# Optimization experiments

Hardware: AMD Instinct MI355X
Metric: run time of the kernel (lower is better)

## Reference

```python
import jax, jax.numpy as jnp
import numpy as np

D_MODEL = 1024
NUM_HEADS = 16
D_K = D_MODEL // NUM_HEADS


def setup_inputs() -> dict:
    key = jax.random.key(0)
    ks = jax.random.split(key, 12)
    B, S = 2, 2048
    s = 1.0 / np.sqrt(D_MODEL)
    inp = {
        'q': jax.random.normal(ks[0], (B, S, D_MODEL), jnp.float32),
        'k': jax.random.normal(ks[1], (B, S, D_MODEL), jnp.float32),
        'v': jax.random.normal(ks[2], (B, S, D_MODEL), jnp.float32),
        'mask': jax.random.randint(ks[3], (B, S, S), 0, 2, jnp.int32),
        'Wq_w': jax.random.normal(ks[4], (D_MODEL, D_MODEL), jnp.float32) * s,
        'Wq_b': jnp.zeros((D_MODEL,), jnp.float32),
        'Wk_w': jax.random.normal(ks[5], (D_MODEL, D_MODEL), jnp.float32) * s,
        'Wk_b': jnp.zeros((D_MODEL,), jnp.float32),
        'Wv_w': jax.random.normal(ks[6], (D_MODEL, D_MODEL), jnp.float32) * s,
        'Wv_b': jnp.zeros((D_MODEL,), jnp.float32),
        'Wo_w': jax.random.normal(ks[7], (D_MODEL, D_MODEL), jnp.float32) * s,
        'Wo_b': jnp.zeros((D_MODEL,), jnp.float32),
    }
    return inp


def reference(q, k, v, mask, Wq_w, Wq_b, Wk_w, Wk_b, Wv_w, Wv_b, Wo_w, Wo_b):
    B, Sq, _ = q.shape
    # torch Linear: x @ W.T + b
    qp = (q @ Wq_w.T + Wq_b).reshape(B, Sq, NUM_HEADS, D_K)
    kp = (k @ Wk_w.T + Wk_b).reshape(B, k.shape[1], NUM_HEADS, D_K)
    vp = (v @ Wv_w.T + Wv_b).reshape(B, v.shape[1], NUM_HEADS, D_K)
    # scores: [B, H, Sq, Sk]
    scores = jnp.einsum('bqhd,bkhd->bhqk', qp, kp) / np.sqrt(D_K).astype(np.float32)
    scores = jnp.where(mask[:, None, :, :] == 0, jnp.float32(-10000.0), scores)
    attn = jax.nn.softmax(scores, axis=-1)
    ctx = jnp.einsum('bhqk,bkhd->bqhd', attn, vp).reshape(B, Sq, D_MODEL)
    return ctx @ Wo_w.T + Wo_b
```

## Files before the change

### kernel.cpp

```cpp
#include <hip/hip_runtime.h>

#define DM   1024
#define HN   16
#define DKH  64
#define SEQ  2048
#define BATCH 2

typedef __attribute__((ext_vector_type(8))) __bf16 bf16x8;
typedef __attribute__((ext_vector_type(4))) float  f32x4;
typedef __attribute__((ext_vector_type(16))) float f32x16;
typedef __attribute__((ext_vector_type(2)))  int   i32x2;

#define AS1 __attribute__((address_space(1)))
#define AS3 __attribute__((address_space(3)))
#define GLL(g, l) __builtin_amdgcn_global_load_lds((const AS1 unsigned int*)(const void*)(g), \
                                                   (AS3 unsigned int*)(void*)(l), 16, 0, 0)

__device__ __forceinline__ unsigned short f2bf(float f) {
  union { float f; unsigned u; } v; v.f = f;
  unsigned u = v.u;
  u += 0x7FFFu + ((u >> 16) & 1u);
  return (unsigned short)(u >> 16);
}

__global__ __launch_bounds__(256) void prep_kernel(
    const float* __restrict__ q, const float* __restrict__ k,
    const float* __restrict__ v,
    const float* __restrict__ Wq, const float* __restrict__ Wk,
    const float* __restrict__ Wv, const float* __restrict__ Wo,
    const int* __restrict__ mask,
    unsigned short* __restrict__ q_bf, unsigned short* __restrict__ k_bf,
    unsigned short* __restrict__ v_bf,
    unsigned short* __restrict__ Wq_bf, unsigned short* __restrict__ Wk_bf,
    unsigned short* __restrict__ Wv_bf, unsigned short* __restrict__ Wo_bf,
    unsigned* __restrict__ pkm) {
  const int bid = blockIdx.x;
  if (bid < 12288) {
    int t = bid >> 12, r = bid & 4095;
    const float* in = (t == 0) ? q : (t == 1) ? k : v;
    unsigned short* out = (t == 0) ? q_bf : (t == 1) ? k_bf : v_bf;
    int i = r * 256 + threadIdx.x;
    float4 f = ((const float4*)in)[i];
    ushort4 o;
    o.x = f2bf(f.x); o.y = f2bf(f.y); o.z = f2bf(f.z); o.w = f2bf(f.w);
    ((ushort4*)out)[i] = o;
  } else if (bid < 16384) {
    int b2 = bid - 12288;
    int t = b2 >> 10, r = b2 & 1023;
    const float* in = (t == 0) ? Wq : (t == 1) ? Wk : (t == 2) ? Wv : Wo;
    unsigned short* out = (t == 0) ? Wq_bf : (t == 1) ? Wk_bf : (t == 2) ? Wv_bf : Wo_bf;
    int i = r * 256 + threadIdx.x;
    float4 f = ((const float4*)in)[i];
    ushort4 o;
    o.x = f2bf(f.x); o.y = f2bf(f.y); o.z = f2bf(f.z); o.w = f2bf(f.w);
    ((ushort4*)out)[i] = o;
  } else {
    int W = (bid - 16384) * 256 + threadIdx.x;
    const int4* base = (const int4*)(mask + (size_t)(W >> 6) * SEQ + (size_t)(W & 63) * 32);
    unsigned bits = 0;
#pragma unroll
    for (int g = 0; g < 8; ++g) {
      int4 m = base[g];
      bits |= (unsigned)(m.x != 0) << (4 * g);
      bits |= (unsigned)(m.y != 0) << (4 * g + 1);
      bits |= (unsigned)(m.z != 0) << (4 * g + 2);
      bits |= (unsigned)(m.w != 0) << (4 * g + 3);
    }
    pkm[W] = bits;
  }
}

__device__ __forceinline__ void gemm_core_pipe(
    const unsigned short* __restrict__ A,
    const unsigned short* __restrict__ W,
    unsigned short* lds,
    f32x4 (&acc)[4][4]) {
  const int tid = threadIdx.x;
  const int wave = tid >> 6, lane = tid & 63;
  const int l15 = lane & 15, quad = lane >> 4;
  const int wr = wave >> 1, wc = wave & 1;

  const int rl = lane >> 2;
  const int cg = (lane & 3) ^ (((rl & 3) + ((rl >> 2) & 3)) & 3);
  const unsigned short* ga = A + (size_t)(wave * 32 + rl) * DM + cg * 8;
  const unsigned short* gb = W + (size_t)(wave * 32 + rl) * DM + cg * 8;
  unsigned short* la = lds + wave * 1024;
  unsigned short* lb = lds + 4096 + wave * 1024;

  const int cfr = (quad ^ (((l15 & 3) + ((l15 >> 2) & 3)) & 3)) * 8;

  auto stage = [&](int ki, int sb) {
    const unsigned short* a = ga + ki * 32;
    const unsigned short* b = gb + ki * 32;
    GLL(a, la + sb);                    GLL(a + (size_t)16 * DM, la + sb + 512);
    GLL(b, lb + sb);                    GLL(b + (size_t)16 * DM, lb + sb + 512);
  };
  auto compute = [&](int sb) {
    const unsigned short* Ab = lds + sb;
    const unsigned short* Bb = lds + sb + 4096;
    bf16x8 af[4], bfr[4];
#pragma unroll
    for (int mt = 0; mt < 4; ++mt)
      af[mt] = *(const bf16x8*)(Ab + (size_t)(wr * 64 + mt * 16 + l15) * 32 + cfr);
#pragma unroll
    for (int nt = 0; nt < 4; ++nt)
      bfr[nt] = *(const bf16x8*)(Bb + (size_t)(wc * 64 + nt * 16 + l15) * 32 + cfr);
#pragma unroll
    for (int mt = 0; mt < 4; ++mt)
#pragma unroll
      for (int nt = 0; nt < 4; ++nt)
        acc[mt][nt] = __builtin_amdgcn_mfma_f32_16x16x32_bf16(af[mt], bfr[nt], acc[mt][nt], 0, 0, 0);
  };

  stage(0, 0);
  stage(1, 8192);
  int sb0 = 0, sb1 = 8192, sb2 = 16384;
#pragma unroll 1
  for (int i = 0; i < DM / 32 - 2; ++i) {
    stage(i + 2, sb2);
    asm volatile("s_waitcnt vmcnt(8)\ns_barrier" ::: "memory");
    compute(sb0);
    asm volatile("s_barrier" ::: "memory");
    int t = sb0; sb0 = sb1; sb1 = sb2; sb2 = t;
  }
  asm volatile("s_waitcnt vmcnt(4)\ns_barrier" ::: "memory");
  compute(sb0);
  asm volatile("s_waitcnt vmcnt(0)\ns_barrier" ::: "memory");
  compute(sb1);
}

__global__ __launch_bounds__(256, 3) void gemm_qkv(
    const unsigned short* __restrict__ Aq, const unsigned short* __restrict__ Ak,
    const unsigned short* __restrict__ Av,
    const unsigned short* __restrict__ Wq, const unsigned short* __restrict__ Wk,
    const unsigned short* __restrict__ Wv,
    const float* __restrict__ bq, const float* __restrict__ bk,
    const float* __restrict__ bv,
    unsigned short* __restrict__ oq, unsigned short* __restrict__ ok,
    unsigned short* __restrict__ ovT) {
  const int z = blockIdx.z;
  const unsigned short* A = (z == 0) ? Aq : (z == 1) ? Ak : Av;
  const unsigned short* W = (z == 0) ? Wq : (z == 1) ? Wk : Wv;
  const float* bias = (z == 0) ? bq : (z == 1) ? bk : bv;

  __shared__ __align__(16) unsigned short lds[24576];

  const int bn = blockIdx.x * 128, bm = blockIdx.y * 128;
  f32x4 acc[4][4] = {};
  gemm_core_pipe(A + (size_t)bm * DM, W + (size_t)bn * DM, lds, acc);

  const int tid = threadIdx.x;
  const int wave = tid >> 6, lane = tid & 63;
  const int l15 = lane & 15, quad = lane >> 4;
  const int wr = wave >> 1, wc = wave & 1;

  if (z != 2) {
    const float qs = (z == 0) ? 0.125f * 1.44269504088896f : 1.0f;
    unsigned short* out = (z == 0) ? oq : ok;
#pragma unroll
    for (int mt = 0; mt < 4; ++mt)
#pragma unroll
      for (int nt = 0; nt < 4; ++nt) {
        int col = bn + wc * 64 + nt * 16 + l15;
        float bb = bias[col];
#pragma unroll
        for (int r = 0; r < 4; ++r) {
          int row = bm + wr * 64 + mt * 16 + quad * 4 + r;
          out[(size_t)row * DM + col] = f2bf((acc[mt][nt][r] + bb) * qs);
        }
      }
  } else {
    unsigned short* LT = lds;
    __syncthreads();
#pragma unroll
    for (int mt = 0; mt < 4; ++mt)
#pragma unroll
      for (int nt = 0; nt < 4; ++nt) {
        int c = wc * 64 + nt * 16 + l15;
        float bb = bias[bn + c];
        int t0 = wr * 64 + mt * 16 + quad * 4;
        ushort4 w4;
        w4.x = f2bf(acc[mt][nt][0] + bb);
        w4.y = f2bf(acc[mt][nt][1] + bb);
        w4.z = f2bf(acc[mt][nt][2] + bb);
        w4.w = f2bf(acc[mt][nt][3] + bb);
        *(ushort4*)(LT + (size_t)c * 136 + t0) = w4;
      }
    __syncthreads();
    const int b = bm >> 11, sbase = bm & (SEQ - 1);
#pragma unroll
    for (int j = 0; j < 8; ++j) {
      int c = wave * 32 + (j >> 1) * 8 + (lane >> 3);
      int tk = (j & 1) * 64 + (lane & 7) * 8;
      bf16x8 vv = *(const bf16x8*)(LT + (size_t)c * 136 + tk);
      int C = bn + c;
      int h = C >> 6, dk = C & 63;
      *(bf16x8*)(ovT + ((size_t)((b * HN + h) * DKH + dk)) * SEQ + sbase + tk) = vv;
    }
  }
}

__global__ __launch_bounds__(256, 3) void gemm_wo(
    const unsigned short* __restrict__ A, const unsigned short* __restrict__ W,
    const float* __restrict__ bias, float* __restrict__ out) {
  __shared__ __align__(16) unsigned short lds[24576];

  const int bn = blockIdx.x * 128, bm = blockIdx.y * 128;
  f32x4 acc[4][4] = {};
  gemm_core_pipe(A + (size_t)bm * DM, W + (size_t)bn * DM, lds, acc);

  const int tid = threadIdx.x;
  const int wave = tid >> 6, lane = tid & 63;
  const int l15 = lane & 15, quad = lane >> 4;
  const int wr = wave >> 1, wc = wave & 1;

#pragma unroll
  for (int mt = 0; mt < 4; ++mt)
#pragma unroll
    for (int nt = 0; nt < 4; ++nt) {
      int col = bn + wc * 64 + nt * 16 + l15;
      float bb = bias[col];
#pragma unroll
      for (int r = 0; r < 4; ++r) {
        int row = bm + wr * 64 + mt * 16 + quad * 4 + r;
        out[(size_t)row * DM + col] = acc[mt][nt][r] + bb;
      }
    }
}

__global__ __launch_bounds__(512, 4) void attn_kernel(
    const unsigned short* __restrict__ qp,
    const unsigned short* __restrict__ kp,
    const unsigned short* __restrict__ vpT,
    const unsigned* __restrict__ pk,
    unsigned short* __restrict__ ctx) {
  const int lane = threadIdx.x & 63;
  const int wave = threadIdx.x >> 6;
  const int wq = wave & 3, wk = wave >> 2;
  const int l31 = lane & 31, hi = lane >> 5, l7 = lane & 7;
  const int bh = blockIdx.x;
  const int b = bh >> 4, h = bh & 15;
  const int qrow = blockIdx.y * 128 + wq * 32 + l31;
  const int kbase = wk << 10;

  __shared__ __align__(16) unsigned short lds[32768];
  unsigned short* G = lds + wk * 16384;

  const unsigned short* qb = qp + ((size_t)(b * SEQ + qrow)) * DM + h * DKH + hi * 8;
  bf16x8 qf[4];
#pragma unroll
  for (int kt = 0; kt < 4; ++kt) qf[kt] = *(const bf16x8*)(qb + kt * 16);

  f32x16 o0 = {}, o1 = {}, lacc = {};
  bf16x8 ones;
#pragma unroll
  for (int i = 0; i < 8; ++i) ones[i] = (__bf16)1.0f;

  const int r8 = lane >> 3;
  const int cg = (l7 ^ r8) * 8;
  const unsigned short* kg0 = kp + ((size_t)(b * SEQ + kbase + wq * 16 + r8)) * DM + h * DKH + cg;
  const unsigned short* kg1 = kg0 + (size_t)8 * DM;
  const unsigned short* vg0 = vpT + ((size_t)(bh * DKH + wq * 16 + r8)) * SEQ + kbase + cg;
  const unsigned short* vg1 = vg0 + (size_t)8 * SEQ;
  unsigned short* lK = G + wq * 1024;
  unsigned short* lV = G + 8192 + wq * 1024;

  int roff[4];
#pragma unroll
  for (int x = 0; x < 4; ++x)
    roff[x] = l31 * 64 + (((x * 2 + hi) ^ l7) * 8);

  const unsigned* mb = pk + (size_t)(b * SEQ + qrow) * (SEQ / 32);

  auto make_pa = [&](const f32x16& sc, bf16x8& paA, bf16x8& paB) {
    float p[16];
#pragma unroll
    for (int r = 0; r < 16; ++r) p[r] = __builtin_amdgcn_exp2f(sc[r]);
    unsigned X0, X1, Y0, Y1;
    asm("v_cvt_pk_bf16_f32 %0, %1, %2" : "=v"(X0) : "v"(p[0]), "v"(p[1]));
    asm("v_cvt_pk_bf16_f32 %0, %1, %2" : "=v"(X1) : "v"(p[2]), "v"(p[3]));
    asm("v_cvt_pk_bf16_f32 %0, %1, %2" : "=v"(Y0) : "v"(p[4]), "v"(p[5]));
    asm("v_cvt_pk_bf16_f32 %0, %1, %2" : "=v"(Y1) : "v"(p[6]), "v"(p[7]));
    i32x2 s0 = __builtin_amdgcn_permlane32_swap((int)X0, (int)Y0, false, false);
    i32x2 s1 = __builtin_amdgcn_permlane32_swap((int)X1, (int)Y1, false, false);
    union { unsigned u[4]; bf16x8 v; } ua;
    ua.u[0] = (unsigned)s0.x; ua.u[1] = (unsigned)s1.x;
    ua.u[2] = (unsigned)s0.y; ua.u[3] = (unsigned)s1.y;
    paA = ua.v;
    asm("v_cvt_pk_bf16_f32 %0, %1, %2" : "=v"(X0) : "v"(p[8]),  "v"(p[9]));
    asm("v_cvt_pk_bf16_f32 %0, %1, %2" : "=v"(X1) : "v"(p[10]), "v"(p[11]));
    asm("v_cvt_pk_bf16_f32 %0, %1, %2" : "=v"(Y0) : "v"(p[12]), "v"(p[13]));
    asm("v_cvt_pk_bf16_f32 %0, %1, %2" : "=v"(Y1) : "v"(p[14]), "v"(p[15]));
    s0 = __builtin_amdgcn_permlane32_swap((int)X0, (int)Y0, false, false);
    s1 = __builtin_amdgcn_permlane32_swap((int)X1, (int)Y1, false, false);
    union { unsigned u[4]; bf16x8 v; } ub;
    ub.u[0] = (unsigned)s0.x; ub.u[1] = (unsigned)s1.x;
    ub.u[2] = (unsigned)s0.y; ub.u[3] = (unsigned)s1.y;
    paB = ub.v;
  };

  auto compute_tile = [&](int kabs, const unsigned short* Kb, const unsigned short* Vb) {
    uint2 mw = *(const uint2*)(mb + (kabs >> 5));
    unsigned bx = mw.x >> (4 * hi);
    unsigned by = mw.y >> (4 * hi);

    f32x16 sc0, sc1;
#pragma unroll
    for (int r = 0; r < 16; ++r) {
      int n = (r & 3) + 8 * (r >> 2);
      sc0[r] = ((bx >> n) & 1u) ? 0.0f : -16384.0f;
      sc1[r] = ((by >> n) & 1u) ? 0.0f : -16384.0f;
    }

#pragma unroll
    for (int kt = 0; kt < 4; ++kt) {
      bf16x8 k0 = *(const bf16x8*)(Kb + roff[kt]);
      bf16x8 k1 = *(const bf16x8*)(Kb + 2048 + roff[kt]);
      sc0 = __builtin_amdgcn_mfma_f32_32x32x16_bf16(k0, qf[kt], sc0, 0, 0, 0);
      sc1 = __builtin_amdgcn_mfma_f32_32x32x16_bf16(k1, qf[kt], sc1, 0, 0, 0);
    }

    bf16x8 pa[4];
    make_pa(sc0, pa[0], pa[1]);
    make_pa(sc1, pa[2], pa[3]);

#pragma unroll
    for (int kc = 0; kc < 4; ++kc)
      lacc = __builtin_amdgcn_mfma_f32_32x32x16_bf16(pa[kc], ones, lacc, 0, 0, 0);

#pragma unroll
    for (int kc = 0; kc < 4; ++kc) {
      bf16x8 v0 = *(const bf16x8*)(Vb + roff[kc]);
      bf16x8 v1 = *(const bf16x8*)(Vb + 2048 + roff[kc]);
      o0 = __builtin_amdgcn_mfma_f32_32x32x16_bf16(pa[kc], v0, o0, 0, 0, 0);
      o1 = __builtin_amdgcn_mfma_f32_32x32x16_bf16(pa[kc], v1, o1, 0, 0, 0);
    }
  };

  GLL(kg0, lK);           GLL(kg1, lK + 512);
  GLL(vg0, lV);           GLL(vg1, lV + 512);

#pragma unroll 1
  for (int j0 = 0; j0 < 1024; j0 += 128) {
    __syncthreads();
    if (j0 + 64 < 1024) {
      GLL(kg0 + (size_t)(j0 + 64) * DM, lK + 4096);
      GLL(kg1 + (size_t)(j0 + 64) * DM, lK + 4096 + 512);
      GLL(vg0 + (j0 + 64), lV + 4096);
      GLL(vg1 + (j0 + 64), lV + 4096 + 512);
    }
    compute_tile(kbase + j0, G, G + 8192);

    __syncthreads();
    if (j0 + 128 < 1024) {
      GLL(kg0 + (size_t)(j0 + 128) * DM, lK);
      GLL(kg1 + (size_t)(j0 + 128) * DM, lK + 512);
      GLL(vg0 + (j0 + 128), lV);
      GLL(vg1 + (j0 + 128), lV + 512);
    }
    compute_tile(kbase + j0 + 64, G + 4096, G + 12288);
  }

  __syncthreads();
  float* cbase = (float*)lds + wq * 3328 + lane * 52;
  if (wk) {
#pragma unroll
    for (int i = 0; i < 4; ++i) {
      f32x4 a, b2, c;
#pragma unroll
      for (int j = 0; j < 4; ++j) {
        a[j] = o0[4 * i + j]; b2[j] = o1[4 * i + j]; c[j] = lacc[4 * i + j];
      }
      *(f32x4*)(cbase + 4 * i)      = a;
      *(f32x4*)(cbase + 16 + 4 * i) = b2;
      *(f32x4*)(cbase + 32 + 4 * i) = c;
    }
  }
  __syncthreads();
  if (!wk) {
#pragma unroll
    for (int i = 0; i < 4; ++i) {
      f32x4 a = *(const f32x4*)(cbase + 4 * i);
      f32x4 b2 = *(const f32x4*)(cbase + 16 + 4 * i);
      f32x4 c = *(const f32x4*)(cbase + 32 + 4 * i);
#pragma unroll
      for (int j = 0; j < 4; ++j) {
        o0[4 * i + j] += a[j]; o1[4 * i + j] += b2[j]; lacc[4 * i + j] += c[j];
      }
    }
    const int qbase = blockIdx.y * 128 + wq * 32;
#pragma unroll
    for (int r = 0; r < 16; ++r) {
      int qg = qbase + (r & 3) + 8 * (r >> 2) + 4 * hi;
      float inv = 1.0f / lacc[r];
      unsigned short* op = ctx + ((size_t)(b * SEQ + qg)) * DM + h * DKH + l31;
      op[0]  = f2bf(o0[r] * inv);
      op[32] = f2bf(o1[r] * inv);
    }
  }
}

extern "C" void kernel_launch(void* const* d_in, const int* in_sizes, int n_in,
                              void* d_out, int out_size, void* d_ws, size_t ws_size,
                              hipStream_t stream) {
  const float* q    = (const float*)d_in[0];
  const float* k    = (const float*)d_in[1];
  const float* v    = (const float*)d_in[2];
  const int*   mask = (const int*)d_in[3];
  const float* Wq_w = (const float*)d_in[4];
  const float* Wq_b = (const float*)d_in[5];
  const float* Wk_w = (const float*)d_in[6];
  const float* Wk_b = (const float*)d_in[7];
  const float* Wv_w = (const float*)d_in[8];
  const float* Wv_b = (const float*)d_in[9];
  const float* Wo_w = (const float*)d_in[10];
  const float* Wo_b = (const float*)d_in[11];

  char* ws = (char*)d_ws;
  const size_t MB = 1024 * 1024;
  unsigned short* q_bf  = (unsigned short*)(ws + 0 * MB);
  unsigned short* k_bf  = (unsigned short*)(ws + 8 * MB);
  unsigned short* v_bf  = (unsigned short*)(ws + 16 * MB);
  unsigned short* Wq_bf = (unsigned short*)(ws + 24 * MB);
  unsigned short* Wk_bf = (unsigned short*)(ws + 26 * MB);
  unsigned short* Wv_bf = (unsigned short*)(ws + 28 * MB);
  unsigned short* Wo_bf = (unsigned short*)(ws + 30 * MB);
  unsigned short* qp    = (unsigned short*)(ws + 32 * MB);
  unsigned short* kp    = (unsigned short*)(ws + 40 * MB);
  unsigned short* vpT   = (unsigned short*)(ws + 48 * MB);
  unsigned short* ctx   = (unsigned short*)(ws + 56 * MB);
  unsigned* pkm = (unsigned*)d_out;

  const int M = BATCH * SEQ;

  prep_kernel<<<17408, 256, 0, stream>>>(q, k, v, Wq_w, Wk_w, Wv_w, Wo_w, mask,
                                         q_bf, k_bf, v_bf, Wq_bf, Wk_bf, Wv_bf,
                                         Wo_bf, pkm);

  gemm_qkv<<<dim3(DM / 128, M / 128, 3), 256, 0, stream>>>(
      q_bf, k_bf, v_bf, Wq_bf, Wk_bf, Wv_bf, Wq_b, Wk_b, Wv_b, qp, kp, vpT);

  attn_kernel<<<dim3(BATCH * HN, SEQ / 128), 512, 0, stream>>>(qp, kp, vpT, pkm, ctx);

  gemm_wo<<<dim3(DM / 128, M / 128), 256, 0, stream>>>(ctx, Wo_bf, Wo_b, (float*)d_out);
}
```

Measured before the change: 137.3 us.

## Process two 32-row query tiles per wave to reuse K/V fragments

Each wave now handles 64 query rows using two sets of Q fragments and accumulators. Every K and V fragment loaded from LDS feeds two MFMAs, which halves LDS reads per unit of compute. The block covers 256 query rows, so the grid is half as large, and launch bounds are relaxed to 2 blocks per SM for register headroom. s_setprio hints are placed around the MFMA sections, and the cross-wave reduction runs in two rounds, which adds barriers. Fewer blocks and higher register use lower occupancy.

```diff
diff --git a/kernel.cpp b/kernel.cpp
--- a/kernel.cpp
+++ b/kernel.cpp
@@ -228,7 +228,7 @@
     }
 }
 
-__global__ __launch_bounds__(512, 4) void attn_kernel(
+__global__ __launch_bounds__(512, 2) void attn_kernel(
     const unsigned short* __restrict__ qp,
     const unsigned short* __restrict__ kp,
     const unsigned short* __restrict__ vpT,
@@ -240,18 +240,22 @@
   const int l31 = lane & 31, hi = lane >> 5, l7 = lane & 7;
   const int bh = blockIdx.x;
   const int b = bh >> 4, h = bh & 15;
-  const int qrow = blockIdx.y * 128 + wq * 32 + l31;
+  const int qbase = blockIdx.y * 256 + wq * 64;
   const int kbase = wk << 10;
 
   __shared__ __align__(16) unsigned short lds[32768];
   unsigned short* G = lds + wk * 16384;
 
-  const unsigned short* qb = qp + ((size_t)(b * SEQ + qrow)) * DM + h * DKH + hi * 8;
-  bf16x8 qf[4];
-#pragma unroll
-  for (int kt = 0; kt < 4; ++kt) qf[kt] = *(const bf16x8*)(qb + kt * 16);
-
-  f32x16 o0 = {}, o1 = {}, lacc = {};
+  const unsigned short* qb0 = qp + ((size_t)(b * SEQ + qbase + l31)) * DM + h * DKH + hi * 8;
+  const unsigned short* qb1 = qb0 + (size_t)32 * DM;
+  bf16x8 qf0[4], qf1[4];
+#pragma unroll
+  for (int kt = 0; kt < 4; ++kt) {
+    qf0[kt] = *(const bf16x8*)(qb0 + kt * 16);
+    qf1[kt] = *(const bf16x8*)(qb1 + kt * 16);
+  }
+
+  f32x16 o00 = {}, o01 = {}, o10 = {}, o11 = {}, lacc0 = {}, lacc1 = {};
   bf16x8 ones;
 #pragma unroll
   for (int i = 0; i < 8; ++i) ones[i] = (__bf16)1.0f;
@@ -270,7 +274,8 @@
   for (int x = 0; x < 4; ++x)
     roff[x] = l31 * 64 + (((x * 2 + hi) ^ l7) * 8);
 
-  const unsigned* mb = pk + (size_t)(b * SEQ + qrow) * (SEQ / 32);
+  const unsigned* mb0 = pk + (size_t)(b * SEQ + qbase + l31) * (SEQ / 32);
+  const unsigned* mb1 = mb0 + (size_t)32 * (SEQ / 32);
 
   auto make_pa = [&](const f32x16& sc, bf16x8& paA, bf16x8& paB) {
     float p[16];
@@ -299,42 +304,55 @@
     paB = ub.v;
   };
 
-  auto compute_tile = [&](int kabs, const unsigned short* Kb, const unsigned short* Vb) {
-    uint2 mw = *(const uint2*)(mb + (kabs >> 5));
-    unsigned bx = mw.x >> (4 * hi);
-    unsigned by = mw.y >> (4 * hi);
-
-    f32x16 sc0, sc1;
+  auto half_tile = [&](unsigned bits0, unsigned bits1, int koff, int kc0,
+                       const unsigned short* Kb, const unsigned short* Vb) {
+    f32x16 sA, sB;
 #pragma unroll
     for (int r = 0; r < 16; ++r) {
       int n = (r & 3) + 8 * (r >> 2);
-      sc0[r] = ((bx >> n) & 1u) ? 0.0f : -16384.0f;
-      sc1[r] = ((by >> n) & 1u) ? 0.0f : -16384.0f;
-    }
-
+      sA[r] = ((bits0 >> n) & 1u) ? 0.0f : -16384.0f;
+      sB[r] = ((bits1 >> n) & 1u) ? 0.0f : -16384.0f;
+    }
+    __builtin_amdgcn_s_setprio(1);
 #pragma unroll
     for (int kt = 0; kt < 4; ++kt) {
-      bf16x8 k0 = *(const bf16x8*)(Kb + roff[kt]);
-      bf16x8 k1 = *(const bf16x8*)(Kb + 2048 + roff[kt]);
-      sc0 = __builtin_amdgcn_mfma_f32_32x32x16_bf16(k0, qf[kt], sc0, 0, 0, 0);
-      sc1 = __builtin_amdgcn_mfma_f32_32x32x16_bf16(k1, qf[kt], sc1, 0, 0, 0);
-    }
-
-    bf16x8 pa[4];
-    make_pa(sc0, pa[0], pa[1]);
-    make_pa(sc1, pa[2], pa[3]);
-
-#pragma unroll
-    for (int kc = 0; kc < 4; ++kc)
-      lacc = __builtin_amdgcn_mfma_f32_32x32x16_bf16(pa[kc], ones, lacc, 0, 0, 0);
-
-#pragma unroll
-    for (int kc = 0; kc < 4; ++kc) {
-      bf16x8 v0 = *(const bf16x8*)(Vb + roff[kc]);
-      bf16x8 v1 = *(const bf16x8*)(Vb + 2048 + roff[kc]);
-      o0 = __builtin_amdgcn_mfma_f32_32x32x16_bf16(pa[kc], v0, o0, 0, 0, 0);
-      o1 = __builtin_amdgcn_mfma_f32_32x32x16_bf16(pa[kc], v1, o1, 0, 0, 0);
-    }
+      bf16x8 kf = *(const bf16x8*)(Kb + koff + roff[kt]);
+      sA = __builtin_amdgcn_mfma_f32_32x32x16_bf16(kf, qf0[kt], sA, 0, 0, 0);
+      sB = __builtin_amdgcn_mfma_f32_32x32x16_bf16(kf, qf1[kt], sB, 0, 0, 0);
+    }
+    __builtin_amdgcn_s_setprio(0);
+    bf16x8 pA0, pA1, pB0, pB1;
+    make_pa(sA, pA0, pA1);
+    make_pa(sB, pB0, pB1);
+    __builtin_amdgcn_s_setprio(1);
+    lacc0 = __builtin_amdgcn_mfma_f32_32x32x16_bf16(pA0, ones, lacc0, 0, 0, 0);
+    lacc0 = __builtin_amdgcn_mfma_f32_32x32x16_bf16(pA1, ones, lacc0, 0, 0, 0);
+    lacc1 = __builtin_amdgcn_mfma_f32_32x32x16_bf16(pB0, ones, lacc1, 0, 0, 0);
+    lacc1 = __builtin_amdgcn_mfma_f32_32x32x16_bf16(pB1, ones, lacc1, 0, 0, 0);
+    {
+      bf16x8 v0 = *(const bf16x8*)(Vb + roff[kc0]);
+      bf16x8 v1 = *(const bf16x8*)(Vb + 2048 + roff[kc0]);
+      o00 = __builtin_amdgcn_mfma_f32_32x32x16_bf16(pA0, v0, o00, 0, 0, 0);
+      o01 = __builtin_amdgcn_mfma_f32_32x32x16_bf16(pA0, v1, o01, 0, 0, 0);
+      o10 = __builtin_amdgcn_mfma_f32_32x32x16_bf16(pB0, v0, o10, 0, 0, 0);
+      o11 = __builtin_amdgcn_mfma_f32_32x32x16_bf16(pB0, v1, o11, 0, 0, 0);
+    }
+    {
+      bf16x8 v0 = *(const bf16x8*)(Vb + roff[kc0 + 1]);
+      bf16x8 v1 = *(const bf16x8*)(Vb + 2048 + roff[kc0 + 1]);
+      o00 = __builtin_amdgcn_mfma_f32_32x32x16_bf16(pA1, v0, o00, 0, 0, 0);
+      o01 = __builtin_amdgcn_mfma_f32_32x32x16_bf16(pA1, v1, o01, 0, 0, 0);
+      o10 = __builtin_amdgcn_mfma_f32_32x32x16_bf16(pB1, v0, o10, 0, 0, 0);
+      o11 = __builtin_amdgcn_mfma_f32_32x32x16_bf16(pB1, v1, o11, 0, 0, 0);
+    }
+    __builtin_amdgcn_s_setprio(0);
+  };
+
+  auto compute_tile = [&](int kabs, const unsigned short* Kb, const unsigned short* Vb) {
+    uint2 mw0 = *(const uint2*)(mb0 + (kabs >> 5));
+    uint2 mw1 = *(const uint2*)(mb1 + (kabs >> 5));
+    half_tile(mw0.x >> (4 * hi), mw1.x >> (4 * hi), 0, 0, Kb, Vb);
+    half_tile(mw0.y >> (4 * hi), mw1.y >> (4 * hi), 2048, 2, Kb, Vb);
   };
 
   GLL(kg0, lK);           GLL(kg1, lK + 512);
@@ -361,41 +379,77 @@
     compute_tile(kbase + j0 + 64, G + 4096, G + 12288);
   }
 
+  float* cb = (float*)lds + ((size_t)(wq * 64 + lane)) * 52;
   __syncthreads();
-  float* cbase = (float*)lds + wq * 3328 + lane * 52;
   if (wk) {
 #pragma unroll
     for (int i = 0; i < 4; ++i) {
       f32x4 a, b2, c;
 #pragma unroll
       for (int j = 0; j < 4; ++j) {
-        a[j] = o0[4 * i + j]; b2[j] = o1[4 * i + j]; c[j] = lacc[4 * i + j];
-      }
-      *(f32x4*)(cbase + 4 * i)      = a;
-      *(f32x4*)(cbase + 16 + 4 * i) = b2;
-      *(f32x4*)(cbase + 32 + 4 * i) = c;
+        a[j] = o00[4 * i + j]; b2[j] = o01[4 * i + j]; c[j] = lacc0[4 * i + j];
+      }
+      *(f32x4*)(cb + 4 * i)      = a;
+      *(f32x4*)(cb + 16 + 4 * i) = b2;
+      *(f32x4*)(cb + 32 + 4 * i) = c;
     }
   }
   __syncthreads();
   if (!wk) {
 #pragma unroll
     for (int i = 0; i < 4; ++i) {
-      f32x4 a = *(const f32x4*)(cbase + 4 * i);
-      f32x4 b2 = *(const f32x4*)(cbase + 16 + 4 * i);
-      f32x4 c = *(const f32x4*)(cbase + 32 + 4 * i);
+      f32x4 a = *(const f32x4*)(cb + 4 * i);
+      f32x4 b2 = *(const f32x4*)(cb + 16 + 4 * i);
+      f32x4 c = *(const f32x4*)(cb + 32 + 4 * i);
 #pragma unroll
       for (int j = 0; j < 4; ++j) {
-        o0[4 * i + j] += a[j]; o1[4 * i + j] += b2[j]; lacc[4 * i + j] += c[j];
-      }
-    }
-    const int qbase = blockIdx.y * 128 + wq * 32;
+        o00[4 * i + j] += a[j]; o01[4 * i + j] += b2[j]; lacc0[4 * i + j] += c[j];
+      }
+    }
+  }
+  __syncthreads();
+  if (wk) {
+#pragma unroll
+    for (int i = 0; i < 4; ++i) {
+      f32x4 a, b2, c;
+#pragma unroll
+      for (int j = 0; j < 4; ++j) {
+        a[j] = o10[4 * i + j]; b2[j] = o11[4 * i + j]; c[j] = lacc1[4 * i + j];
+      }
+      *(f32x4*)(cb + 4 * i)      = a;
+      *(f32x4*)(cb + 16 + 4 * i) = b2;
+      *(f32x4*)(cb + 32 + 4 * i) = c;
+    }
+  }
+  __syncthreads();
+  if (!wk) {
+#pragma unroll
+    for (int i = 0; i < 4; ++i) {
+      f32x4 a = *(const f32x4*)(cb + 4 * i);
+      f32x4 b2 = *(const f32x4*)(cb + 16 + 4 * i);
+      f32x4 c = *(const f32x4*)(cb + 32 + 4 * i);
+#pragma unroll
+      for (int j = 0; j < 4; ++j) {
+        o10[4 * i + j] += a[j]; o11[4 * i + j] += b2[j]; lacc1[4 * i + j] += c[j];
+      }
+    }
 #pragma unroll
     for (int r = 0; r < 16; ++r) {
-      int qg = qbase + (r & 3) + 8 * (r >> 2) + 4 * hi;
-      float inv = 1.0f / lacc[r];
-      unsigned short* op = ctx + ((size_t)(b * SEQ + qg)) * DM + h * DKH + l31;
-      op[0]  = f2bf(o0[r] * inv);
-      op[32] = f2bf(o1[r] * inv);
+      int qoff = (r & 3) + 8 * (r >> 2) + 4 * hi;
+      {
+        int qg = qbase + qoff;
+        float inv = 1.0f / lacc0[r];
+        unsigned short* op = ctx + ((size_t)(b * SEQ + qg)) * DM + h * DKH + l31;
+        op[0]  = f2bf(o00[r] * inv);
+        op[32] = f2bf(o01[r] * inv);
+      }
+      {
+        int qg = qbase + 32 + qoff;
+        float inv = 1.0f / lacc1[r];
+        unsigned short* op = ctx + ((size_t)(b * SEQ + qg)) * DM + h * DKH + l31;
+        op[0]  = f2bf(o10[r] * inv);
+        op[32] = f2bf(o11[r] * inv);
+      }
     }
   }
 }
@@ -440,7 +494,7 @@
   gemm_qkv<<<dim3(DM / 128, M / 128, 3), 256, 0, stream>>>(
       q_bf, k_bf, v_bf, Wq_bf, Wk_bf, Wv_bf, Wq_b, Wk_b, Wv_b, qp, kp, vpT);
 
-  attn_kernel<<<dim3(BATCH * HN, SEQ / 128), 512, 0, stream>>>(qp, kp, vpT, pkm, ctx);
+  attn_kernel<<<dim3(BATCH * HN, SEQ / 256), 512, 0, stream>>>(qp, kp, vpT, pkm, ctx);
 
   gemm_wo<<<dim3(DM / 128, M / 128), 256, 0, stream>>>(ctx, Wo_bf, Wo_b, (float*)d_out);
 }
```

After: 137.3 us. About the same (-0.0%).

## Deepen K/V prefetch pipeline with manual vmcnt waits and MFMA priority

Applied to the files above, without the earlier changes.

Restructures the attention inner loop so that two K/V tiles are in flight at once. Hand-written s_waitcnt vmcnt/s_barrier sequences replace the __syncthreads calls, so a barrier no longer drains every outstanding load. Mask words are now loaded one tile ahead into registers instead of being read inside the compute step. s_setprio is raised around the MFMA blocks so the matrix instructions are favoured during scheduling. The risk is correctness: the vmcnt counts must exactly match the number of outstanding global loads, and the changed iteration count has to cover the same key range.

```diff
diff --git a/kernel.cpp b/kernel.cpp
--- a/kernel.cpp
+++ b/kernel.cpp
@@ -270,7 +270,7 @@
   for (int x = 0; x < 4; ++x)
     roff[x] = l31 * 64 + (((x * 2 + hi) ^ l7) * 8);
 
-  const unsigned* mb = pk + (size_t)(b * SEQ + qrow) * (SEQ / 32);
+  const uint2* mb2 = (const uint2*)(pk + (size_t)(b * SEQ + qrow) * (SEQ / 32) + (kbase >> 5));
 
   auto make_pa = [&](const f32x16& sc, bf16x8& paA, bf16x8& paB) {
     float p[16];
@@ -299,8 +299,7 @@
     paB = ub.v;
   };
 
-  auto compute_tile = [&](int kabs, const unsigned short* Kb, const unsigned short* Vb) {
-    uint2 mw = *(const uint2*)(mb + (kabs >> 5));
+  auto compute_tile = [&](uint2 mw, const unsigned short* Kb, const unsigned short* Vb) {
     unsigned bx = mw.x >> (4 * hi);
     unsigned by = mw.y >> (4 * hi);
 
@@ -312,6 +311,7 @@
       sc1[r] = ((by >> n) & 1u) ? 0.0f : -16384.0f;
     }
 
+    __builtin_amdgcn_s_setprio(1);
 #pragma unroll
     for (int kt = 0; kt < 4; ++kt) {
       bf16x8 k0 = *(const bf16x8*)(Kb + roff[kt]);
@@ -319,11 +319,13 @@
       sc0 = __builtin_amdgcn_mfma_f32_32x32x16_bf16(k0, qf[kt], sc0, 0, 0, 0);
       sc1 = __builtin_amdgcn_mfma_f32_32x32x16_bf16(k1, qf[kt], sc1, 0, 0, 0);
     }
+    __builtin_amdgcn_s_setprio(0);
 
     bf16x8 pa[4];
     make_pa(sc0, pa[0], pa[1]);
     make_pa(sc1, pa[2], pa[3]);
 
+    __builtin_amdgcn_s_setprio(1);
 #pragma unroll
     for (int kc = 0; kc < 4; ++kc)
       lacc = __builtin_amdgcn_mfma_f32_32x32x16_bf16(pa[kc], ones, lacc, 0, 0, 0);
@@ -335,31 +337,33 @@
       o0 = __builtin_amdgcn_mfma_f32_32x32x16_bf16(pa[kc], v0, o0, 0, 0, 0);
       o1 = __builtin_amdgcn_mfma_f32_32x32x16_bf16(pa[kc], v1, o1, 0, 0, 0);
     }
+    __builtin_amdgcn_s_setprio(0);
   };
 
-  GLL(kg0, lK);           GLL(kg1, lK + 512);
-  GLL(vg0, lV);           GLL(vg1, lV + 512);
-
+  GLL(kg0, lK);                        GLL(kg1, lK + 512);
+  GLL(vg0, lV);                        GLL(vg1, lV + 512);
+  uint2 mA = mb2[0];
+  GLL(kg0 + (size_t)64 * DM, lK + 4096); GLL(kg1 + (size_t)64 * DM, lK + 4096 + 512);
+  GLL(vg0 + 64, lV + 4096);              GLL(vg1 + 64, lV + 4096 + 512);
+  uint2 mB = mb2[1];
+
+  int sa = 0;
 #pragma unroll 1
-  for (int j0 = 0; j0 < 1024; j0 += 128) {
-    __syncthreads();
-    if (j0 + 64 < 1024) {
-      GLL(kg0 + (size_t)(j0 + 64) * DM, lK + 4096);
-      GLL(kg1 + (size_t)(j0 + 64) * DM, lK + 4096 + 512);
-      GLL(vg0 + (j0 + 64), lV + 4096);
-      GLL(vg1 + (j0 + 64), lV + 4096 + 512);
-    }
-    compute_tile(kbase + j0, G, G + 8192);
-
-    __syncthreads();
-    if (j0 + 128 < 1024) {
-      GLL(kg0 + (size_t)(j0 + 128) * DM, lK);
-      GLL(kg1 + (size_t)(j0 + 128) * DM, lK + 512);
-      GLL(vg0 + (j0 + 128), lV);
-      GLL(vg1 + (j0 + 128), lV + 512);
-    }
-    compute_tile(kbase + j0 + 64, G + 4096, G + 12288);
-  }
+  for (int j = 0; j < 14; ++j) {
+    asm volatile("s_waitcnt vmcnt(5)\ns_barrier" ::: "memory");
+    compute_tile(mA, G + sa, G + 8192 + sa);
+    asm volatile("s_barrier" ::: "memory");
+    size_t ko = (size_t)(j + 2) * 64;
+    GLL(kg0 + ko * DM, lK + sa);      GLL(kg1 + ko * DM, lK + sa + 512);
+    GLL(vg0 + ko, lV + sa);           GLL(vg1 + ko, lV + sa + 512);
+    mA = mB;  mB = mb2[j + 2];
+    sa ^= 4096;
+  }
+  asm volatile("s_waitcnt vmcnt(5)\ns_barrier" ::: "memory");
+  compute_tile(mA, G + sa, G + 8192 + sa);
+  sa ^= 4096;
+  asm volatile("s_waitcnt vmcnt(0)\ns_barrier" ::: "memory");
+  compute_tile(mB, G + sa, G + 8192 + sa);
 
   __syncthreads();
   float* cbase = (float*)lds + wq * 3328 + lane * 52;
```

Result: no change. 135.7 us (-1.2%).

## Load V fragments directly from global memory and raise priority around MFMA blocks

Applied to the files above, without the earlier changes.

V tiles are no longer staged through LDS with global_load_lds. Each lane now reads its transposed-V fragments straight from global memory into registers inside compute_tile. This removes the LDS traffic and bandwidth spent on V. s_setprio is also raised around the MFMA sections so waves issuing matrix ops get scheduling preference. In exchange, the per-tile global V loads are no longer prefetched a tile ahead, so their latency may be exposed, and V is now re-read from global/L2 by every wave that shares a tile.

```diff
diff --git a/kernel.cpp b/kernel.cpp
--- a/kernel.cpp
+++ b/kernel.cpp
@@ -260,15 +260,15 @@
   const int cg = (l7 ^ r8) * 8;
   const unsigned short* kg0 = kp + ((size_t)(b * SEQ + kbase + wq * 16 + r8)) * DM + h * DKH + cg;
   const unsigned short* kg1 = kg0 + (size_t)8 * DM;
-  const unsigned short* vg0 = vpT + ((size_t)(bh * DKH + wq * 16 + r8)) * SEQ + kbase + cg;
-  const unsigned short* vg1 = vg0 + (size_t)8 * SEQ;
   unsigned short* lK = G + wq * 1024;
-  unsigned short* lV = G + 8192 + wq * 1024;
 
   int roff[4];
 #pragma unroll
   for (int x = 0; x < 4; ++x)
     roff[x] = l31 * 64 + (((x * 2 + hi) ^ l7) * 8);
+
+  const unsigned short* vb0 = vpT + ((size_t)(bh * DKH + l31)) * SEQ + kbase + hi * 8;
+  const unsigned short* vb1 = vb0 + (size_t)32 * SEQ;
 
   const unsigned* mb = pk + (size_t)(b * SEQ + qrow) * (SEQ / 32);
 
@@ -299,7 +299,7 @@
     paB = ub.v;
   };
 
-  auto compute_tile = [&](int kabs, const unsigned short* Kb, const unsigned short* Vb) {
+  auto compute_tile = [&](int kabs, int jt, const unsigned short* Kb) {
     uint2 mw = *(const uint2*)(mb + (kabs >> 5));
     unsigned bx = mw.x >> (4 * hi);
     unsigned by = mw.y >> (4 * hi);
@@ -312,6 +312,7 @@
       sc1[r] = ((by >> n) & 1u) ? 0.0f : -16384.0f;
     }
 
+    __builtin_amdgcn_s_setprio(1);
 #pragma unroll
     for (int kt = 0; kt < 4; ++kt) {
       bf16x8 k0 = *(const bf16x8*)(Kb + roff[kt]);
@@ -319,26 +320,33 @@
       sc0 = __builtin_amdgcn_mfma_f32_32x32x16_bf16(k0, qf[kt], sc0, 0, 0, 0);
       sc1 = __builtin_amdgcn_mfma_f32_32x32x16_bf16(k1, qf[kt], sc1, 0, 0, 0);
     }
+    __builtin_amdgcn_s_setprio(0);
+
+    bf16x8 v0[4], v1[4];
+#pragma unroll
+    for (int kc = 0; kc < 4; ++kc) {
+      v0[kc] = *(const bf16x8*)(vb0 + jt * 64 + kc * 16);
+      v1[kc] = *(const bf16x8*)(vb1 + jt * 64 + kc * 16);
+    }
 
     bf16x8 pa[4];
     make_pa(sc0, pa[0], pa[1]);
     make_pa(sc1, pa[2], pa[3]);
 
+    __builtin_amdgcn_s_setprio(1);
 #pragma unroll
     for (int kc = 0; kc < 4; ++kc)
       lacc = __builtin_amdgcn_mfma_f32_32x32x16_bf16(pa[kc], ones, lacc, 0, 0, 0);
 
 #pragma unroll
     for (int kc = 0; kc < 4; ++kc) {
-      bf16x8 v0 = *(const bf16x8*)(Vb + roff[kc]);
-      bf16x8 v1 = *(const bf16x8*)(Vb + 2048 + roff[kc]);
-      o0 = __builtin_amdgcn_mfma_f32_32x32x16_bf16(pa[kc], v0, o0, 0, 0, 0);
-      o1 = __builtin_amdgcn_mfma_f32_32x32x16_bf16(pa[kc], v1, o1, 0, 0, 0);
-    }
+      o0 = __builtin_amdgcn_mfma_f32_32x32x16_bf16(pa[kc], v0[kc], o0, 0, 0, 0);
+      o1 = __builtin_amdgcn_mfma_f32_32x32x16_bf16(pa[kc], v1[kc], o1, 0, 0, 0);
+    }
+    __builtin_amdgcn_s_setprio(0);
   };
 
   GLL(kg0, lK);           GLL(kg1, lK + 512);
-  GLL(vg0, lV);           GLL(vg1, lV + 512);
 
 #pragma unroll 1
   for (int j0 = 0; j0 < 1024; j0 += 128) {
@@ -346,19 +354,15 @@
     if (j0 + 64 < 1024) {
       GLL(kg0 + (size_t)(j0 + 64) * DM, lK + 4096);
       GLL(kg1 + (size_t)(j0 + 64) * DM, lK + 4096 + 512);
-      GLL(vg0 + (j0 + 64), lV + 4096);
-      GLL(vg1 + (j0 + 64), lV + 4096 + 512);
-    }
-    compute_tile(kbase + j0, G, G + 8192);
+    }
+    compute_tile(kbase + j0, j0 >> 6, G);
 
     __syncthreads();
     if (j0 + 128 < 1024) {
       GLL(kg0 + (size_t)(j0 + 128) * DM, lK);
       GLL(kg1 + (size_t)(j0 + 128) * DM, lK + 512);
-      GLL(vg0 + (j0 + 128), lV);
-      GLL(vg1 + (j0 + 128), lV + 512);
-    }
-    compute_tile(kbase + j0 + 64, G + 4096, G + 12288);
+    }
+    compute_tile(kbase + j0 + 64, (j0 >> 6) + 1, G + 4096);
   }
 
   __syncthreads();
```

Result: slower. 296.4 us (+115.8%).
